# Performance work log

Measured on AMD Instinct MI355X. Metric: run time of the kernel, lower is better.

Reference implementation:

```python
import jax, jax.numpy as jnp
import numpy as np

B, S, H, I = 2, 1024, 1024, 4096
G, E = 4, 4
NE = G * E
CAP = 1024


def setup_inputs() -> dict:
    key = jax.random.key(0)
    ks = jax.random.split(key, 6)
    return {
        "hidden_states": jax.random.normal(ks[0], (B, S, H), jnp.float32),
        "group_router_w": jax.random.normal(ks[1], (G, H), jnp.float32) * 0.02,
        "expert_router_w": jax.random.normal(ks[2], (G, E, H), jnp.float32) * 0.02,
        "gate_w": jax.random.normal(ks[3], (NE, I, H), jnp.float32) * 0.02,
        "up_w": jax.random.normal(ks[4], (NE, I, H), jnp.float32) * 0.02,
        "down_w": jax.random.normal(ks[5], (NE, H, I), jnp.float32) * 0.02,
    }


def _forward(x, gw, erw, Wg, Wu, Wd):
    b, s, h = x.shape
    T = b * s
    xf = x.reshape(T, h)
    # level 1: group routing (fp32 softmax, top-2 groups)
    group_logits = xf @ gw.T                                        # [T,G]
    group_probs = jax.nn.softmax(group_logits.astype(jnp.float32), axis=-1)
    top_gp, top_gi = jax.lax.top_k(group_probs, 2)                  # [T,2]
    # level 2: per-group expert routing (top-1 expert within group)
    expert_logits = jnp.einsum('th,geh->tge', xf, erw)              # [T,G,E]
    expert_probs = jax.nn.softmax(expert_logits.astype(jnp.float32), axis=-1)
    e_idx = jnp.argmax(expert_probs, axis=-1)                       # [T,G]
    e_prob = jnp.max(expert_probs, axis=-1)                         # [T,G]
    sel_e = jnp.take_along_axis(e_idx, top_gi, axis=1)              # [T,2]
    sel_p = jnp.take_along_axis(e_prob, top_gi, axis=1)             # [T,2]
    eid = (top_gi * E + sel_e).reshape(-1)                          # [2T] global expert id
    wgt = (top_gp * sel_p).reshape(-1)                              # [2T] combine weight
    x2 = jnp.repeat(xf, 2, axis=0)                                  # [2T,H], slot-major per token
    # capacity-based dispatch: position within expert via cumsum of one-hot
    onehot = jax.nn.one_hot(eid, NE, dtype=jnp.int32)               # [2T,NE]
    pos = (jnp.cumsum(onehot, axis=0) * onehot).sum(axis=1) - 1     # [2T]
    keep = pos < CAP
    pos_c = jnp.where(keep, pos, CAP)                               # overflow -> dummy slot
    buf = jnp.zeros((NE, CAP + 1, h), x.dtype).at[eid, pos_c].set(x2)
    # grouped-GEMM gated FFN (SwiGLU) over all experts at once
    gate = jax.nn.silu(jnp.einsum('ech,eih->eci', buf, Wg))
    up = jnp.einsum('ech,eih->eci', buf, Wu)
    yexp = jnp.einsum('eci,ehi->ech', gate * up, Wd)                # [NE,CAP+1,H]
    # combine: gather back and weight; dropped tokens get zero weight
    y = yexp[eid, pos_c] * jnp.where(keep, wgt, 0.0)[:, None].astype(x.dtype)
    out = (y[0::2] + y[1::2]).reshape(b, s, h)
    aux_loss = jnp.zeros((), jnp.float32)  # aux-loss accumulation truncated in source; initialized to 0
    return out, aux_loss


def reference(hidden_states, group_router_w, expert_router_w, gate_w, up_w, down_w):
    return _forward(hidden_states, group_router_w, expert_router_w, gate_w, up_w, down_w)
```

## Files before the change

kernel.cpp:

```cpp
#include <hip/hip_runtime.h>
#include <hip/hip_bf16.h>

typedef float f32x4 __attribute__((ext_vector_type(4)));
typedef __bf16 bf16x8 __attribute__((ext_vector_type(8)));

#define H 1024
#define II 4096
#define NE 16
#define CAP 1024
#define NTOK 2048
#define NSLOT 4096

__device__ __forceinline__ void gload16(const void* g, void* l) {
  __builtin_amdgcn_global_load_lds(
      (const __attribute__((address_space(1))) unsigned*)g,
      (__attribute__((address_space(3))) unsigned*)l, 16, 0, 0);
}

__global__ __launch_bounds__(256) void k_route(
    const float* __restrict__ x, const float* __restrict__ gw,
    const float* __restrict__ erw, int* __restrict__ eid,
    float* __restrict__ wgt) {
  int t = blockIdx.x * 4 + (threadIdx.x >> 6);
  int lane = threadIdx.x & 63;
  const float* xr = x + (size_t)t * H;
  double acc[20];
#pragma unroll
  for (int j = 0; j < 20; j++) acc[j] = 0.0;
  for (int it = 0; it < 16; ++it) {
    int h = it * 64 + lane;
    float xv = xr[h];
#pragma unroll
    for (int g = 0; g < 4; ++g) acc[g] += (double)xv * (double)gw[g * H + h];
#pragma unroll
    for (int j = 0; j < 16; ++j)
      acc[4 + j] += (double)xv * (double)erw[j * H + h];
  }
#pragma unroll
  for (int j = 0; j < 20; ++j) {
    double v = acc[j];
#pragma unroll
    for (int o = 32; o > 0; o >>= 1) v += __shfl_down(v, o, 64);
    acc[j] = v;
  }
  if (lane == 0) {
    float gl[4];
#pragma unroll
    for (int g = 0; g < 4; g++) gl[g] = (float)acc[g];
    int g1 = 0;
#pragma unroll
    for (int g = 1; g < 4; g++)
      if (gl[g] > gl[g1]) g1 = g;
    int g2 = (g1 == 0) ? 1 : 0;
#pragma unroll
    for (int g = 0; g < 4; g++)
      if (g != g1 && gl[g] > gl[g2]) g2 = g;
    float gm = fmaxf(fmaxf(gl[0], gl[1]), fmaxf(gl[2], gl[3]));
    float s = 0.f;
#pragma unroll
    for (int g = 0; g < 4; g++) s += expf(gl[g] - gm);
    float p[2] = {expf(gl[g1] - gm) / s, expf(gl[g2] - gm) / s};
    int gs[2] = {g1, g2};
#pragma unroll
    for (int k = 0; k < 2; k++) {
      int g = gs[k];
      float el[4];
#pragma unroll
      for (int e2 = 0; e2 < 4; e2++) el[e2] = (float)acc[4 + g * 4 + e2];
      int eb = 0;
#pragma unroll
      for (int e2 = 1; e2 < 4; e2++)
        if (el[e2] > el[eb]) eb = e2;
      float es = 0.f;
#pragma unroll
      for (int e2 = 0; e2 < 4; e2++) es += expf(el[e2] - el[eb]);
      eid[2 * t + k] = g * 4 + eb;
      wgt[2 * t + k] = p[k] * (1.f / es);
    }
  }
}

__global__ __launch_bounds__(1024) void k_scan(const int* __restrict__ eid,
                                               int* __restrict__ perm,
                                               int* __restrict__ cnt,
                                               int* __restrict__ kept) {
  int wid = threadIdx.x >> 6;
  int lane = threadIdx.x & 63;
  int base = 0;
  for (int it = 0; it < 64; ++it) {
    int slot = it * 64 + lane;
    int e = eid[slot];
    unsigned long long m = __ballot(e == wid);
    if (e == wid) {
      int pos = base + __popcll(m & ((1ull << lane) - 1ull));
      if (pos < CAP) {
        perm[wid * CAP + pos] = slot;
        kept[slot] = 1;
      } else {
        kept[slot] = 0;
      }
    }
    base += __popcll(m);
  }
  if (lane == 0) cnt[wid] = (base < CAP) ? base : CAP;
}

__global__ __launch_bounds__(256) void k_gateup(
    const float* __restrict__ x, const float* __restrict__ Wg,
    const float* __restrict__ Wu, const int* __restrict__ perm,
    const int* __restrict__ cnt, __bf16* __restrict__ act) {
  __shared__ float As[128 * 32];
  __shared__ float Gs[64 * 32];
  __shared__ float Us[64 * 32];
  __shared__ int slotArr[128];
  const int e = blockIdx.z, nt = blockIdx.x, rt = blockIdx.y;
  const int ce = cnt[e];
  if (rt * 128 >= ce) return;
  const int tid = threadIdx.x, lane = tid & 63, wid = tid >> 6;
  if (tid < 128) {
    int ridx = rt * 128 + tid;
    slotArr[tid] = perm[e * CAP + (ridx < ce ? ridx : 0)];
  }
  __syncthreads();
  int tokA[4], offA[4];
#pragma unroll
  for (int q = 0; q < 4; q++) {
    int r = wid * 32 + q * 8 + (lane >> 3);
    tokA[q] = slotArr[r] >> 1;
    offA[q] = (((lane & 7) ^ (r & 7))) * 4;
  }
  int rowW[2], offW[2];
#pragma unroll
  for (int q = 0; q < 2; q++) {
    int r = wid * 16 + q * 8 + (lane >> 3);
    rowW[q] = r;
    offW[q] = (((lane & 7) ^ (r & 7))) * 4;
  }
  const size_t ew = (size_t)e * II * H;
  const float* Wge = Wg + ew + (size_t)(nt * 64) * H;
  const float* Wue = Wu + ew + (size_t)(nt * 64) * H;
  const int wm = wid >> 1, wn = wid & 1;

  f32x4 accG[4][2], accU[4][2];
#pragma unroll
  for (int m = 0; m < 4; m++)
#pragma unroll
    for (int n = 0; n < 2; n++)
#pragma unroll
      for (int i = 0; i < 4; i++) {
        accG[m][n][i] = 0.f;
        accU[m][n][i] = 0.f;
      }

  for (int ks = 0; ks < 32; ++ks) {
    const int kb = ks * 32;
#pragma unroll
    for (int q = 0; q < 4; q++)
      gload16(x + (size_t)tokA[q] * H + kb + offA[q],
              &As[(wid * 32 + q * 8) * 32]);
#pragma unroll
    for (int q = 0; q < 2; q++) {
      gload16(Wge + (size_t)rowW[q] * H + kb + offW[q],
              &Gs[(wid * 16 + q * 8) * 32]);
      gload16(Wue + (size_t)rowW[q] * H + kb + offW[q],
              &Us[(wid * 16 + q * 8) * 32]);
    }
    __syncthreads();
    bf16x8 aF[4], gF[2], uF[2];
#pragma unroll
    for (int m = 0; m < 4; m++) {
      int r = wm * 64 + m * 16 + (lane & 15);
      int c0 = 2 * (lane >> 4);
      f32x4 lo = *(const f32x4*)&As[r * 32 + ((c0) ^ (r & 7)) * 4];
      f32x4 hi = *(const f32x4*)&As[r * 32 + ((c0 + 1) ^ (r & 7)) * 4];
      bf16x8 f;
#pragma unroll
      for (int i = 0; i < 4; i++) {
        f[i] = (__bf16)lo[i];
        f[i + 4] = (__bf16)hi[i];
      }
      aF[m] = f;
    }
#pragma unroll
    for (int n = 0; n < 2; n++) {
      int r = wn * 32 + n * 16 + (lane & 15);
      int c0 = 2 * (lane >> 4);
      {
        f32x4 lo = *(const f32x4*)&Gs[r * 32 + ((c0) ^ (r & 7)) * 4];
        f32x4 hi = *(const f32x4*)&Gs[r * 32 + ((c0 + 1) ^ (r & 7)) * 4];
        bf16x8 f;
#pragma unroll
        for (int i = 0; i < 4; i++) {
          f[i] = (__bf16)lo[i];
          f[i + 4] = (__bf16)hi[i];
        }
        gF[n] = f;
      }
      {
        f32x4 lo = *(const f32x4*)&Us[r * 32 + ((c0) ^ (r & 7)) * 4];
        f32x4 hi = *(const f32x4*)&Us[r * 32 + ((c0 + 1) ^ (r & 7)) * 4];
        bf16x8 f;
#pragma unroll
        for (int i = 0; i < 4; i++) {
          f[i] = (__bf16)lo[i];
          f[i + 4] = (__bf16)hi[i];
        }
        uF[n] = f;
      }
    }
#pragma unroll
    for (int m = 0; m < 4; m++)
#pragma unroll
      for (int n = 0; n < 2; n++) {
        accG[m][n] = __builtin_amdgcn_mfma_f32_16x16x32_bf16(aF[m], gF[n],
                                                             accG[m][n], 0, 0, 0);
        accU[m][n] = __builtin_amdgcn_mfma_f32_16x16x32_bf16(aF[m], uF[n],
                                                             accU[m][n], 0, 0, 0);
      }
    __syncthreads();
  }
  const int colB = nt * 64 + wn * 32;
#pragma unroll
  for (int m = 0; m < 4; m++)
#pragma unroll
    for (int n = 0; n < 2; n++)
#pragma unroll
      for (int i = 0; i < 4; i++) {
        int row = wm * 64 + m * 16 + (lane >> 4) * 4 + i;
        if (rt * 128 + row < ce) {
          int slot = slotArr[row];
          float g = accG[m][n][i];
          float u = accU[m][n][i];
          float a = (g / (1.f + __expf(-g))) * u;
          act[(size_t)slot * II + colB + n * 16 + (lane & 15)] = (__bf16)a;
        }
      }
}

__global__ __launch_bounds__(256) void k_down(
    const __bf16* __restrict__ act, const float* __restrict__ Wd,
    const int* __restrict__ perm, const int* __restrict__ cnt,
    const float* __restrict__ wgt, float* __restrict__ y) {
  __shared__ __bf16 As[128 * 64];
  __shared__ float Ws[64 * 64];
  __shared__ int slotArr[128];
  const int e = blockIdx.z, nt = blockIdx.x, rt = blockIdx.y;
  const int ce = cnt[e];
  if (rt * 128 >= ce) return;
  const int tid = threadIdx.x, lane = tid & 63, wid = tid >> 6;
  if (tid < 128) {
    int ridx = rt * 128 + tid;
    slotArr[tid] = perm[e * CAP + (ridx < ce ? ridx : 0)];
  }
  __syncthreads();
  int slotA[4], offA[4];
#pragma unroll
  for (int q = 0; q < 4; q++) {
    int r = wid * 32 + q * 8 + (lane >> 3);
    slotA[q] = slotArr[r];
    offA[q] = (((lane & 7) ^ (r & 7))) * 8;
  }
  int rowW[4], offW[4];
#pragma unroll
  for (int q = 0; q < 4; q++) {
    int r = wid * 16 + q * 4 + (lane >> 4);
    rowW[q] = r;
    offW[q] = (((lane & 15) ^ (r & 7))) * 4;
  }
  const float* Wde = Wd + (size_t)e * H * II + (size_t)(nt * 64) * II;
  const int wm = wid >> 1, wn = wid & 1;
  f32x4 acc[4][2];
#pragma unroll
  for (int m = 0; m < 4; m++)
#pragma unroll
    for (int n = 0; n < 2; n++)
#pragma unroll
      for (int i = 0; i < 4; i++) acc[m][n][i] = 0.f;

  for (int ks = 0; ks < 64; ++ks) {
    const int kb = ks * 64;
#pragma unroll
    for (int q = 0; q < 4; q++)
      gload16(act + (size_t)slotA[q] * II + kb + offA[q],
              &As[(wid * 32 + q * 8) * 64]);
#pragma unroll
    for (int q = 0; q < 4; q++)
      gload16(Wde + (size_t)rowW[q] * II + kb + offW[q],
              &Ws[(wid * 16 + q * 4) * 64]);
    __syncthreads();
#pragma unroll
    for (int kk = 0; kk < 2; kk++) {
      bf16x8 aF[4], wF[2];
#pragma unroll
      for (int m = 0; m < 4; m++) {
        int r = wm * 64 + m * 16 + (lane & 15);
        int c = (kk * 4 + (lane >> 4)) ^ (r & 7);
        aF[m] = *(const bf16x8*)&As[r * 64 + c * 8];
      }
#pragma unroll
      for (int n = 0; n < 2; n++) {
        int r = wn * 32 + n * 16 + (lane & 15);
        int c0 = kk * 8 + (lane >> 4) * 2;
        f32x4 lo = *(const f32x4*)&Ws[r * 64 + ((c0) ^ (r & 7)) * 4];
        f32x4 hi = *(const f32x4*)&Ws[r * 64 + ((c0 + 1) ^ (r & 7)) * 4];
        bf16x8 f;
#pragma unroll
        for (int i = 0; i < 4; i++) {
          f[i] = (__bf16)lo[i];
          f[i + 4] = (__bf16)hi[i];
        }
        wF[n] = f;
      }
#pragma unroll
      for (int m = 0; m < 4; m++)
#pragma unroll
        for (int n = 0; n < 2; n++)
          acc[m][n] = __builtin_amdgcn_mfma_f32_16x16x32_bf16(aF[m], wF[n],
                                                              acc[m][n], 0, 0, 0);
    }
    __syncthreads();
  }
  const int colB = nt * 64 + wn * 32;
#pragma unroll
  for (int m = 0; m < 4; m++)
#pragma unroll
    for (int n = 0; n < 2; n++)
#pragma unroll
      for (int i = 0; i < 4; i++) {
        int row = wm * 64 + m * 16 + (lane >> 4) * 4 + i;
        if (rt * 128 + row < ce) {
          int slot = slotArr[row];
          y[(size_t)slot * H + colB + n * 16 + (lane & 15)] =
              wgt[slot] * acc[m][n][i];
        }
      }
}

__global__ __launch_bounds__(256) void k_combine(const float* __restrict__ y,
                                                 const int* __restrict__ kept,
                                                 float* __restrict__ out) {
  int t = blockIdx.x, tid = threadIdx.x;
  const f32x4* y0 = (const f32x4*)(y + (size_t)(2 * t) * H);
  const f32x4* y1 = (const f32x4*)(y + (size_t)(2 * t + 1) * H);
  f32x4 a, b;
#pragma unroll
  for (int i = 0; i < 4; i++) {
    a[i] = 0.f;
    b[i] = 0.f;
  }
  if (kept[2 * t]) a = y0[tid];
  if (kept[2 * t + 1]) b = y1[tid];
  ((f32x4*)out)[(size_t)t * 256 + tid] = a + b;
  if (t == 0 && tid == 0) out[(size_t)NTOK * H] = 0.f;
}

extern "C" void kernel_launch(void* const* d_in, const int* in_sizes, int n_in,
                              void* d_out, int out_size, void* d_ws,
                              size_t ws_size, hipStream_t stream) {
  const float* x = (const float*)d_in[0];
  const float* gw = (const float*)d_in[1];
  const float* erw = (const float*)d_in[2];
  const float* Wg = (const float*)d_in[3];
  const float* Wu = (const float*)d_in[4];
  const float* Wd = (const float*)d_in[5];
  float* out = (float*)d_out;
  char* ws = (char*)d_ws;
  int* eid = (int*)(ws);
  float* wgt = (float*)(ws + (16 << 10));
  int* kept = (int*)(ws + (32 << 10));
  int* cnt = (int*)(ws + (48 << 10));
  int* perm = (int*)(ws + (64 << 10));
  __bf16* act = (__bf16*)(ws + (128 << 10));
  float* yb = (float*)(ws + (128 << 10) + (size_t)NSLOT * II * 2);

  k_route<<<NTOK / 4, 256, 0, stream>>>(x, gw, erw, eid, wgt);
  k_scan<<<1, 1024, 0, stream>>>(eid, perm, cnt, kept);
  k_gateup<<<dim3(64, 8, 16), 256, 0, stream>>>(x, Wg, Wu, perm, cnt, act);
  k_down<<<dim3(16, 8, 16), 256, 0, stream>>>(act, Wd, perm, cnt, wgt, yb);
  k_combine<<<NTOK, 256, 0, stream>>>(yb, kept, out);
}
```

Baseline: 420.1 us.

## Pre-convert activations to bf16, double-buffer register-staged GEMM tiles, widen down tile

A new kernel converts the input x to bf16 once, so gate/up loads half the activation bytes and skips the repeated per-tile conversion. Both expert GEMMs drop direct global-to-LDS loads for register-staged loads that convert fp32 weights to bf16 before writing LDS. They now use double-buffered shared memory, prefetching the next K tile while MFMAs run on the current one. The down-projection tile widens from 64 to 128 output columns per block, giving more reuse per activation load. The cost is more registers and LDS, lower occupancy, one extra launch, and conversion ALU moved onto the load path.

```diff
diff --git a/kernel.cpp b/kernel.cpp
--- a/kernel.cpp
+++ b/kernel.cpp
@@ -10,12 +10,6 @@
 #define CAP 1024
 #define NTOK 2048
 #define NSLOT 4096
-
-__device__ __forceinline__ void gload16(const void* g, void* l) {
-  __builtin_amdgcn_global_load_lds(
-      (const __attribute__((address_space(1))) unsigned*)g,
-      (__attribute__((address_space(3))) unsigned*)l, 16, 0, 0);
-}
 
 __global__ __launch_bounds__(256) void k_route(
     const float* __restrict__ x, const float* __restrict__ gw,
@@ -105,13 +99,27 @@
   if (lane == 0) cnt[wid] = (base < CAP) ? base : CAP;
 }
 
+__global__ __launch_bounds__(256) void k_cvtx(const float* __restrict__ x,
+                                              __bf16* __restrict__ xb) {
+  size_t i = ((size_t)blockIdx.x * 256 + threadIdx.x) * 8;
+  f32x4 a = *(const f32x4*)(x + i);
+  f32x4 b = *(const f32x4*)(x + i + 4);
+  bf16x8 o;
+#pragma unroll
+  for (int j = 0; j < 4; j++) {
+    o[j] = (__bf16)a[j];
+    o[j + 4] = (__bf16)b[j];
+  }
+  *(bf16x8*)(xb + i) = o;
+}
+
 __global__ __launch_bounds__(256) void k_gateup(
-    const float* __restrict__ x, const float* __restrict__ Wg,
+    const __bf16* __restrict__ xb, const float* __restrict__ Wg,
     const float* __restrict__ Wu, const int* __restrict__ perm,
     const int* __restrict__ cnt, __bf16* __restrict__ act) {
-  __shared__ float As[128 * 32];
-  __shared__ float Gs[64 * 32];
-  __shared__ float Us[64 * 32];
+  __shared__ __bf16 As[2][128 * 64];
+  __shared__ __bf16 Gs[2][64 * 64];
+  __shared__ __bf16 Us[2][64 * 64];
   __shared__ int slotArr[128];
   const int e = blockIdx.z, nt = blockIdx.x, rt = blockIdx.y;
   const int ce = cnt[e];
@@ -122,25 +130,28 @@
     slotArr[tid] = perm[e * CAP + (ridx < ce ? ridx : 0)];
   }
   __syncthreads();
-  int tokA[4], offA[4];
+  const int srow = tid >> 3;
+  const int sch = tid & 7;
+  const __bf16* pA[4];
+  int wrA[4];
 #pragma unroll
   for (int q = 0; q < 4; q++) {
-    int r = wid * 32 + q * 8 + (lane >> 3);
-    tokA[q] = slotArr[r] >> 1;
-    offA[q] = (((lane & 7) ^ (r & 7))) * 4;
-  }
-  int rowW[2], offW[2];
+    int r = q * 32 + srow;
+    pA[q] = xb + (size_t)(slotArr[r] >> 1) * H + sch * 8;
+    wrA[q] = r * 64 + (sch ^ (r & 7)) * 8;
+  }
+  const size_t ew = (size_t)e * II * H + (size_t)(nt * 64) * H;
+  const float* pG[2];
+  const float* pU[2];
+  int wrW[2];
 #pragma unroll
   for (int q = 0; q < 2; q++) {
-    int r = wid * 16 + q * 8 + (lane >> 3);
-    rowW[q] = r;
-    offW[q] = (((lane & 7) ^ (r & 7))) * 4;
-  }
-  const size_t ew = (size_t)e * II * H;
-  const float* Wge = Wg + ew + (size_t)(nt * 64) * H;
-  const float* Wue = Wu + ew + (size_t)(nt * 64) * H;
+    int r = q * 32 + srow;
+    pG[q] = Wg + ew + (size_t)r * H + sch * 8;
+    pU[q] = Wu + ew + (size_t)r * H + sch * 8;
+    wrW[q] = r * 64 + (sch ^ (r & 7)) * 8;
+  }
   const int wm = wid >> 1, wn = wid & 1;
-
   f32x4 accG[4][2], accU[4][2];
 #pragma unroll
   for (int m = 0; m < 4; m++)
@@ -151,72 +162,94 @@
         accG[m][n][i] = 0.f;
         accU[m][n][i] = 0.f;
       }
-
-  for (int ks = 0; ks < 32; ++ks) {
-    const int kb = ks * 32;
-#pragma unroll
-    for (int q = 0; q < 4; q++)
-      gload16(x + (size_t)tokA[q] * H + kb + offA[q],
-              &As[(wid * 32 + q * 8) * 32]);
+  {
+    bf16x8 va[4];
+    f32x4 g0[2], g1[2], u0[2], u1[2];
+#pragma unroll
+    for (int q = 0; q < 4; q++) va[q] = *(const bf16x8*)(pA[q]);
 #pragma unroll
     for (int q = 0; q < 2; q++) {
-      gload16(Wge + (size_t)rowW[q] * H + kb + offW[q],
-              &Gs[(wid * 16 + q * 8) * 32]);
-      gload16(Wue + (size_t)rowW[q] * H + kb + offW[q],
-              &Us[(wid * 16 + q * 8) * 32]);
-    }
-    __syncthreads();
-    bf16x8 aF[4], gF[2], uF[2];
-#pragma unroll
-    for (int m = 0; m < 4; m++) {
-      int r = wm * 64 + m * 16 + (lane & 15);
-      int c0 = 2 * (lane >> 4);
-      f32x4 lo = *(const f32x4*)&As[r * 32 + ((c0) ^ (r & 7)) * 4];
-      f32x4 hi = *(const f32x4*)&As[r * 32 + ((c0 + 1) ^ (r & 7)) * 4];
-      bf16x8 f;
+      g0[q] = *(const f32x4*)(pG[q]);
+      g1[q] = *(const f32x4*)(pG[q] + 4);
+      u0[q] = *(const f32x4*)(pU[q]);
+      u1[q] = *(const f32x4*)(pU[q] + 4);
+    }
+#pragma unroll
+    for (int q = 0; q < 4; q++) *(bf16x8*)&As[0][wrA[q]] = va[q];
+#pragma unroll
+    for (int q = 0; q < 2; q++) {
+      bf16x8 fg, fu;
 #pragma unroll
       for (int i = 0; i < 4; i++) {
-        f[i] = (__bf16)lo[i];
-        f[i + 4] = (__bf16)hi[i];
-      }
-      aF[m] = f;
-    }
-#pragma unroll
-    for (int n = 0; n < 2; n++) {
-      int r = wn * 32 + n * 16 + (lane & 15);
-      int c0 = 2 * (lane >> 4);
-      {
-        f32x4 lo = *(const f32x4*)&Gs[r * 32 + ((c0) ^ (r & 7)) * 4];
-        f32x4 hi = *(const f32x4*)&Gs[r * 32 + ((c0 + 1) ^ (r & 7)) * 4];
-        bf16x8 f;
+        fg[i] = (__bf16)g0[q][i];
+        fg[i + 4] = (__bf16)g1[q][i];
+        fu[i] = (__bf16)u0[q][i];
+        fu[i + 4] = (__bf16)u1[q][i];
+      }
+      *(bf16x8*)&Gs[0][wrW[q]] = fg;
+      *(bf16x8*)&Us[0][wrW[q]] = fu;
+    }
+  }
+  __syncthreads();
+  for (int t = 0; t < 16; ++t) {
+    const int cb = t & 1, nb = cb ^ 1;
+    bf16x8 va[4];
+    f32x4 g0[2], g1[2], u0[2], u1[2];
+    if (t < 15) {
+      const int ko = (t + 1) * 64;
+#pragma unroll
+      for (int q = 0; q < 4; q++) va[q] = *(const bf16x8*)(pA[q] + ko);
+#pragma unroll
+      for (int q = 0; q < 2; q++) {
+        g0[q] = *(const f32x4*)(pG[q] + ko);
+        g1[q] = *(const f32x4*)(pG[q] + ko + 4);
+        u0[q] = *(const f32x4*)(pU[q] + ko);
+        u1[q] = *(const f32x4*)(pU[q] + ko + 4);
+      }
+    }
+#pragma unroll
+    for (int kk = 0; kk < 2; ++kk) {
+      bf16x8 aF[4], gF[2], uF[2];
+#pragma unroll
+      for (int m = 0; m < 4; m++) {
+        int r = wm * 64 + m * 16 + (lane & 15);
+        int c = (kk * 4 + (lane >> 4)) ^ (r & 7);
+        aF[m] = *(const bf16x8*)&As[cb][r * 64 + c * 8];
+      }
+#pragma unroll
+      for (int n = 0; n < 2; n++) {
+        int rg = wn * 32 + n * 16 + (lane & 15);
+        int c = (kk * 4 + (lane >> 4)) ^ (rg & 7);
+        gF[n] = *(const bf16x8*)&Gs[cb][rg * 64 + c * 8];
+        uF[n] = *(const bf16x8*)&Us[cb][rg * 64 + c * 8];
+      }
+#pragma unroll
+      for (int m = 0; m < 4; m++)
+#pragma unroll
+        for (int n = 0; n < 2; n++) {
+          accG[m][n] = __builtin_amdgcn_mfma_f32_16x16x32_bf16(
+              aF[m], gF[n], accG[m][n], 0, 0, 0);
+          accU[m][n] = __builtin_amdgcn_mfma_f32_16x16x32_bf16(
+              aF[m], uF[n], accU[m][n], 0, 0, 0);
+        }
+    }
+    if (t < 15) {
+#pragma unroll
+      for (int q = 0; q < 4; q++) *(bf16x8*)&As[nb][wrA[q]] = va[q];
+#pragma unroll
+      for (int q = 0; q < 2; q++) {
+        bf16x8 fg, fu;
 #pragma unroll
         for (int i = 0; i < 4; i++) {
-          f[i] = (__bf16)lo[i];
-          f[i + 4] = (__bf16)hi[i];
+          fg[i] = (__bf16)g0[q][i];
+          fg[i + 4] = (__bf16)g1[q][i];
+          fu[i] = (__bf16)u0[q][i];
+          fu[i + 4] = (__bf16)u1[q][i];
         }
-        gF[n] = f;
-      }
-      {
-        f32x4 lo = *(const f32x4*)&Us[r * 32 + ((c0) ^ (r & 7)) * 4];
-        f32x4 hi = *(const f32x4*)&Us[r * 32 + ((c0 + 1) ^ (r & 7)) * 4];
-        bf16x8 f;
-#pragma unroll
-        for (int i = 0; i < 4; i++) {
-          f[i] = (__bf16)lo[i];
-          f[i + 4] = (__bf16)hi[i];
-        }
-        uF[n] = f;
-      }
-    }
-#pragma unroll
-    for (int m = 0; m < 4; m++)
-#pragma unroll
-      for (int n = 0; n < 2; n++) {
-        accG[m][n] = __builtin_amdgcn_mfma_f32_16x16x32_bf16(aF[m], gF[n],
-                                                             accG[m][n], 0, 0, 0);
-        accU[m][n] = __builtin_amdgcn_mfma_f32_16x16x32_bf16(aF[m], uF[n],
-                                                             accU[m][n], 0, 0, 0);
-      }
+        *(bf16x8*)&Gs[nb][wrW[q]] = fg;
+        *(bf16x8*)&Us[nb][wrW[q]] = fu;
+      }
+    }
     __syncthreads();
   }
   const int colB = nt * 64 + wn * 32;
@@ -241,8 +274,8 @@
     const __bf16* __restrict__ act, const float* __restrict__ Wd,
     const int* __restrict__ perm, const int* __restrict__ cnt,
     const float* __restrict__ wgt, float* __restrict__ y) {
-  __shared__ __bf16 As[128 * 64];
-  __shared__ float Ws[64 * 64];
+  __shared__ __bf16 As[2][128 * 64];
+  __shared__ __bf16 Ws[2][128 * 64];
   __shared__ int slotArr[128];
   const int e = blockIdx.z, nt = blockIdx.x, rt = blockIdx.y;
   const int ce = cnt[e];
@@ -253,78 +286,103 @@
     slotArr[tid] = perm[e * CAP + (ridx < ce ? ridx : 0)];
   }
   __syncthreads();
-  int slotA[4], offA[4];
+  const int srow = tid >> 3;
+  const int sch = tid & 7;
+  const __bf16* pA[4];
+  const float* pW[4];
+  int wrA[4];
 #pragma unroll
   for (int q = 0; q < 4; q++) {
-    int r = wid * 32 + q * 8 + (lane >> 3);
-    slotA[q] = slotArr[r];
-    offA[q] = (((lane & 7) ^ (r & 7))) * 8;
-  }
-  int rowW[4], offW[4];
-#pragma unroll
-  for (int q = 0; q < 4; q++) {
-    int r = wid * 16 + q * 4 + (lane >> 4);
-    rowW[q] = r;
-    offW[q] = (((lane & 15) ^ (r & 7))) * 4;
-  }
-  const float* Wde = Wd + (size_t)e * H * II + (size_t)(nt * 64) * II;
+    int r = q * 32 + srow;
+    pA[q] = act + (size_t)slotArr[r] * II + sch * 8;
+    pW[q] = Wd + (size_t)e * H * II + (size_t)(nt * 128 + r) * II + sch * 8;
+    wrA[q] = r * 64 + (sch ^ (r & 7)) * 8;
+  }
   const int wm = wid >> 1, wn = wid & 1;
-  f32x4 acc[4][2];
+  f32x4 acc[4][4];
 #pragma unroll
   for (int m = 0; m < 4; m++)
 #pragma unroll
-    for (int n = 0; n < 2; n++)
+    for (int n = 0; n < 4; n++)
 #pragma unroll
       for (int i = 0; i < 4; i++) acc[m][n][i] = 0.f;
-
-  for (int ks = 0; ks < 64; ++ks) {
-    const int kb = ks * 64;
-#pragma unroll
-    for (int q = 0; q < 4; q++)
-      gload16(act + (size_t)slotA[q] * II + kb + offA[q],
-              &As[(wid * 32 + q * 8) * 64]);
-#pragma unroll
-    for (int q = 0; q < 4; q++)
-      gload16(Wde + (size_t)rowW[q] * II + kb + offW[q],
-              &Ws[(wid * 16 + q * 4) * 64]);
-    __syncthreads();
-#pragma unroll
-    for (int kk = 0; kk < 2; kk++) {
-      bf16x8 aF[4], wF[2];
+  {
+    bf16x8 va[4];
+    f32x4 w0[4], w1[4];
+#pragma unroll
+    for (int q = 0; q < 4; q++) {
+      va[q] = *(const bf16x8*)(pA[q]);
+      w0[q] = *(const f32x4*)(pW[q]);
+      w1[q] = *(const f32x4*)(pW[q] + 4);
+    }
+#pragma unroll
+    for (int q = 0; q < 4; q++) {
+      *(bf16x8*)&As[0][wrA[q]] = va[q];
+      bf16x8 fw;
+#pragma unroll
+      for (int i = 0; i < 4; i++) {
+        fw[i] = (__bf16)w0[q][i];
+        fw[i + 4] = (__bf16)w1[q][i];
+      }
+      *(bf16x8*)&Ws[0][wrA[q]] = fw;
+    }
+  }
+  __syncthreads();
+  for (int t = 0; t < 64; ++t) {
+    const int cb = t & 1, nb = cb ^ 1;
+    bf16x8 va[4];
+    f32x4 w0[4], w1[4];
+    if (t < 63) {
+      const int ko = (t + 1) * 64;
+#pragma unroll
+      for (int q = 0; q < 4; q++) {
+        va[q] = *(const bf16x8*)(pA[q] + ko);
+        w0[q] = *(const f32x4*)(pW[q] + ko);
+        w1[q] = *(const f32x4*)(pW[q] + ko + 4);
+      }
+    }
+#pragma unroll
+    for (int kk = 0; kk < 2; ++kk) {
+      bf16x8 aF[4], wF[4];
 #pragma unroll
       for (int m = 0; m < 4; m++) {
         int r = wm * 64 + m * 16 + (lane & 15);
         int c = (kk * 4 + (lane >> 4)) ^ (r & 7);
-        aF[m] = *(const bf16x8*)&As[r * 64 + c * 8];
-      }
-#pragma unroll
-      for (int n = 0; n < 2; n++) {
-        int r = wn * 32 + n * 16 + (lane & 15);
-        int c0 = kk * 8 + (lane >> 4) * 2;
-        f32x4 lo = *(const f32x4*)&Ws[r * 64 + ((c0) ^ (r & 7)) * 4];
-        f32x4 hi = *(const f32x4*)&Ws[r * 64 + ((c0 + 1) ^ (r & 7)) * 4];
-        bf16x8 f;
-#pragma unroll
-        for (int i = 0; i < 4; i++) {
-          f[i] = (__bf16)lo[i];
-          f[i + 4] = (__bf16)hi[i];
-        }
-        wF[n] = f;
+        aF[m] = *(const bf16x8*)&As[cb][r * 64 + c * 8];
+      }
+#pragma unroll
+      for (int n = 0; n < 4; n++) {
+        int rw = wn * 64 + n * 16 + (lane & 15);
+        int c = (kk * 4 + (lane >> 4)) ^ (rw & 7);
+        wF[n] = *(const bf16x8*)&Ws[cb][rw * 64 + c * 8];
       }
 #pragma unroll
       for (int m = 0; m < 4; m++)
 #pragma unroll
-        for (int n = 0; n < 2; n++)
+        for (int n = 0; n < 4; n++)
           acc[m][n] = __builtin_amdgcn_mfma_f32_16x16x32_bf16(aF[m], wF[n],
                                                               acc[m][n], 0, 0, 0);
     }
+    if (t < 63) {
+#pragma unroll
+      for (int q = 0; q < 4; q++) {
+        *(bf16x8*)&As[nb][wrA[q]] = va[q];
+        bf16x8 fw;
+#pragma unroll
+        for (int i = 0; i < 4; i++) {
+          fw[i] = (__bf16)w0[q][i];
+          fw[i + 4] = (__bf16)w1[q][i];
+        }
+        *(bf16x8*)&Ws[nb][wrA[q]] = fw;
+      }
+    }
     __syncthreads();
   }
-  const int colB = nt * 64 + wn * 32;
+  const int colB = nt * 128 + wn * 64;
 #pragma unroll
   for (int m = 0; m < 4; m++)
 #pragma unroll
-    for (int n = 0; n < 2; n++)
+    for (int n = 0; n < 4; n++)
 #pragma unroll
       for (int i = 0; i < 4; i++) {
         int row = wm * 64 + m * 16 + (lane >> 4) * 4 + i;
@@ -372,10 +430,13 @@
   int* perm = (int*)(ws + (64 << 10));
   __bf16* act = (__bf16*)(ws + (128 << 10));
   float* yb = (float*)(ws + (128 << 10) + (size_t)NSLOT * II * 2);
+  __bf16* xb = (__bf16*)(ws + (128 << 10) + (size_t)NSLOT * II * 2 +
+                         (size_t)NSLOT * H * 4);
 
   k_route<<<NTOK / 4, 256, 0, stream>>>(x, gw, erw, eid, wgt);
   k_scan<<<1, 1024, 0, stream>>>(eid, perm, cnt, kept);
-  k_gateup<<<dim3(64, 8, 16), 256, 0, stream>>>(x, Wg, Wu, perm, cnt, act);
-  k_down<<<dim3(16, 8, 16), 256, 0, stream>>>(act, Wd, perm, cnt, wgt, yb);
+  k_cvtx<<<NTOK * H / 8 / 256, 256, 0, stream>>>(x, xb);
+  k_gateup<<<dim3(64, 8, 16), 256, 0, stream>>>(xb, Wg, Wu, perm, cnt, act);
+  k_down<<<dim3(8, 8, 16), 256, 0, stream>>>(act, Wd, perm, cnt, wgt, yb);
   k_combine<<<NTOK, 256, 0, stream>>>(yb, kept, out);
 }
```

After: 376.7 us. -10.3%, faster.
